# Kernel tuning notes

Measured on AMD Instinct MI355X. Metric: run time of the kernel, lower is better.

Reference implementation:

```python
import jax, jax.numpy as jnp
import numpy as np

B, T, F, D, NCLS = 32, 1024, 128, 64, 11
EPS = 1e-3  # keras BatchNormalization default epsilon


def sinusoidal_pe(t, f, dtype=jnp.float32):
    pos = jnp.arange(t, dtype=jnp.float32)[:, None]                      # [T,1]
    div = jnp.exp(-jnp.log(10000.0) * jnp.arange(0, f, 2, dtype=jnp.float32) / f)
    ang = pos * div                                                      # [T,F/2]
    pe = jnp.zeros((t, f), dtype=jnp.float32)
    pe = pe.at[:, 0::2].set(jnp.sin(ang)).at[:, 1::2].set(jnp.cos(ang))
    return pe.astype(dtype)


def setup_inputs() -> dict:
    key = jax.random.key(0)
    ks = jax.random.split(key, 18)
    s = 0.05
    return {
        "x": jax.random.normal(ks[0], (B, T, F), jnp.float32),
        "wq": jax.random.normal(ks[1], (F, D), jnp.float32) * s,
        "wk": jax.random.normal(ks[2], (F, D), jnp.float32) * s,
        "wv": jax.random.normal(ks[3], (F, D), jnp.float32) * s,
        "bn_a_gamma": jax.random.uniform(ks[4], (D,), jnp.float32, 0.5, 1.5),
        "bn_a_beta": jax.random.normal(ks[5], (D,), jnp.float32) * s,
        "bn_a_mean": jax.random.normal(ks[6], (D,), jnp.float32) * s,
        "bn_a_var": jax.random.uniform(ks[7], (D,), jnp.float32, 0.5, 1.5),
        "w0": jax.random.normal(ks[8], (D, 64), jnp.float32) * s,
        "b0": jax.random.normal(ks[9], (64,), jnp.float32) * s,
        "w1": jax.random.normal(ks[10], (F, 64), jnp.float32) * s,
        "b1": jax.random.normal(ks[11], (64,), jnp.float32) * s,
        "bn1_gamma": jax.random.uniform(ks[12], (128,), jnp.float32, 0.5, 1.5),
        "bn1_beta": jax.random.normal(ks[13], (128,), jnp.float32) * s,
        "bn1_mean": jax.random.normal(ks[14], (128,), jnp.float32) * s,
        "bn1_var": jax.random.uniform(ks[15], (128,), jnp.float32, 0.5, 1.5),
        "wd": jax.random.normal(ks[16], (128, NCLS), jnp.float32) * s,
        "bd": jax.random.normal(ks[17], (NCLS,), jnp.float32) * s,
    }


def _bn(h, gamma, beta, mean, var):
    # inference-mode batch norm over last axis
    return (h - mean) * (gamma * jax.lax.rsqrt(var + EPS)) + beta


def reference(x, wq, wk, wv, bn_a_gamma, bn_a_beta, bn_a_mean, bn_a_var,
              w0, b0, w1, b1, bn1_gamma, bn1_beta, bn1_mean, bn1_var, wd, bd):
    # AttentionLayer: positional encoding + single-head scaled dot-product attention
    xp = x + sinusoidal_pe(x.shape[1], x.shape[2], x.dtype)              # [B,T,F]
    q = jnp.einsum("btf,fd->btd", xp, wq)
    k = jnp.einsum("btf,fd->btd", xp, wk)
    v = jnp.einsum("btf,fd->btd", xp, wv)
    scores = jnp.einsum("bqd,bkd->bqk", q, k) / jnp.sqrt(jnp.float32(D))  # [B,T,T]
    attn = jax.nn.softmax(scores, axis=-1)
    x1 = jnp.einsum("bqk,bkd->bqd", attn, v)                             # [B,T,D]
    x1 = _bn(x1, bn_a_gamma, bn_a_beta, bn_a_mean, bn_a_var)
    # per-timestep heads (vectorized over T)
    out1 = jax.nn.relu(jnp.einsum("btd,de->bte", x1, w0) + b0)           # [B,T,64]
    out2 = jax.nn.relu(jnp.einsum("btf,fe->bte", x, w1) + b1)            # [B,T,64]
    h = jnp.concatenate([out1, out2], axis=-1)                           # [B,T,128]
    h = _bn(h, bn1_gamma, bn1_beta, bn1_mean, bn1_var)
    # dropout is identity in inference mode
    logits = jnp.einsum("bte,ec->btc", h, wd) + bd                       # [B,T,11]
    return jax.nn.softmax(logits, axis=-1)
```

## Files before the change

kernel.cpp:

```cpp
#include <hip/hip_runtime.h>
#include <math.h>

#define BB 32
#define TT 1024
#define FF 128
#define DD 64
#define NCLS 11
constexpr float kEps = 1e-3f;
constexpr int M = BB * TT;

typedef __attribute__((ext_vector_type(8))) short short8v;
typedef __attribute__((ext_vector_type(4))) short short4v;
typedef __attribute__((ext_vector_type(4))) float float4v;
typedef __attribute__((ext_vector_type(16))) float float16v;

__device__ __forceinline__ short f2bf(float f) {
  union { float f; unsigned u; } v; v.f = f;
  return (short)((v.u + 0x7FFFu + ((v.u >> 16) & 1u)) >> 16);
}
__device__ __forceinline__ float bf2f(short s) {
  union { unsigned u; float f; } v; v.u = ((unsigned)(unsigned short)s) << 16;
  return v.f;
}

__device__ __forceinline__ short8v pack_swap(
    float p0, float p1, float p2, float p3,
    float p4, float p5, float p6, float p7) {
  unsigned a0, a1, b0, b1;
  asm("v_cvt_pk_bf16_f32 %0, %1, %2" : "=v"(a0) : "v"(p0), "v"(p1));
  asm("v_cvt_pk_bf16_f32 %0, %1, %2" : "=v"(a1) : "v"(p2), "v"(p3));
  asm("v_cvt_pk_bf16_f32 %0, %1, %2" : "=v"(b0) : "v"(p4), "v"(p5));
  asm("v_cvt_pk_bf16_f32 %0, %1, %2" : "=v"(b1) : "v"(p6), "v"(p7));
  asm volatile("v_permlane32_swap_b32 %0, %1" : "+v"(a0), "+v"(b0));
  asm volatile("v_permlane32_swap_b32 %0, %1" : "+v"(a1), "+v"(b1));
  union { unsigned u[4]; short8v s; } r;
  r.u[0] = a0; r.u[1] = a1; r.u[2] = b0; r.u[3] = b1;
  return r.s;
}

__global__ __launch_bounds__(256) void prep_kernel(
    const float* __restrict__ wq, const float* __restrict__ wk,
    const float* __restrict__ wv, const float* __restrict__ w1,
    const float* __restrict__ w0, const float* __restrict__ b0,
    const float* __restrict__ bn_a_gamma, const float* __restrict__ bn_a_beta,
    const float* __restrict__ bn_a_mean, const float* __restrict__ bn_a_var,
    const float* __restrict__ bn1_gamma, const float* __restrict__ bn1_beta,
    const float* __restrict__ bn1_mean, const float* __restrict__ bn1_var,
    const float* __restrict__ wd, const float* __restrict__ bd,
    short* __restrict__ wT4,
    short* __restrict__ w0pT, float* __restrict__ b0p,
    short* __restrict__ wdpT, float* __restrict__ bdp,
    float* __restrict__ peq, float* __restrict__ pek, float* __restrict__ pev) {
  const int t = threadIdx.x;
  const int blk = blockIdx.x;

  if (blk >= 5) {
    __shared__ float peL[16][128];
    const int p = blk - 5;
    const int y = p >> 6;
    const int t0 = (p & 63) * 16;
#pragma unroll
    for (int i = 0; i < 8; ++i) {
      const int idx = t + i * 256;
      const int tr = idx >> 7, f = idx & 127;
      const float div = expf(-logf(10000.0f) * (float)(f & ~1) / (float)FF);
      const float ang = (float)(t0 + tr) * div;
      peL[tr][f] = (f & 1) ? cosf(ang) : sinf(ang);
    }
    __syncthreads();
    const float* w = (y == 0) ? wq : (y == 1) ? wk : wv;
    float* dst = (y == 0) ? peq : (y == 1) ? pek : pev;
    const int tr = t >> 4, dq = t & 15;
    float4 acc = {0.f, 0.f, 0.f, 0.f};
    for (int f = 0; f < FF; ++f) {
      const float pv = peL[tr][f];
      const float4 w4 = *(const float4*)&w[f * 64 + dq * 4];
      acc.x += pv * w4.x; acc.y += pv * w4.y;
      acc.z += pv * w4.z; acc.w += pv * w4.w;
    }
    *(float4*)&dst[(t0 + tr) * 64 + dq * 4] = acc;
    return;
  }
  if (blk > 0) {
    const int y = blk - 1;
    const float* w = (y == 0) ? wq : (y == 1) ? wk : (y == 2) ? wv : w1;
    short* dst = wT4 + y * 8192;
#pragma unroll
    for (int i = 0; i < 4; ++i) {
      const int idx = t + i * 256;
      const int n = idx >> 4, c = idx & 15;
      short8v s8;
#pragma unroll
      for (int j = 0; j < 8; ++j) s8[j] = f2bf(w[(c * 8 + j) * 64 + n]);
      *(short8v*)&dst[n * 128 + ((c ^ (n & 7)) << 3)] = s8;
    }
    return;
  }
  __shared__ float cA[64], cAo[64], c1s[64], c1o[64], c2s[64], c2o[64];
  if (t < 64) {
    const float sA = bn_a_gamma[t] * rsqrtf(bn_a_var[t] + kEps);
    cA[t] = sA; cAo[t] = bn_a_beta[t] - bn_a_mean[t] * sA;
    const float s1 = bn1_gamma[t] * rsqrtf(bn1_var[t] + kEps);
    c1s[t] = s1; c1o[t] = bn1_beta[t] - bn1_mean[t] * s1;
    const float s2 = bn1_gamma[t + 64] * rsqrtf(bn1_var[t + 64] + kEps);
    c2s[t] = s2; c2o[t] = bn1_beta[t + 64] - bn1_mean[t + 64] * s2;
  }
  __syncthreads();
  for (int i = t; i < 4096; i += 256) {
    const int e = i >> 6, k = i & 63;
    w0pT[i] = f2bf(cA[k] * w0[k * 64 + e]);
  }
  if (t < 64) {
    float s = b0[t];
    for (int k = 0; k < 64; ++k) s += cAo[k] * w0[k * 64 + t];
    b0p[t] = s;
  }
  for (int i = t; i < 2048; i += 256) {
    const int c = i >> 7, e = i & 127;
    float v = 0.f;
    if (c < NCLS) v = wd[e * NCLS + c] * (e < 64 ? c1s[e] : c2s[e - 64]);
    wdpT[i] = f2bf(v);
  }
  if (t < 16) {
    float s = 0.f;
    if (t < NCLS) {
      s = bd[t];
      for (int e = 0; e < 64; ++e) s += c1o[e] * wd[e * NCLS + t];
      for (int e = 0; e < 64; ++e) s += c2o[e] * wd[(64 + e) * NCLS + t];
    }
    bdp[t] = s;
  }
}

__global__ __launch_bounds__(256) void proj_kernel(
    const float* __restrict__ x, const short* __restrict__ wT4,
    const float* __restrict__ peq, const float* __restrict__ pek,
    const float* __restrict__ pev, const float* __restrict__ b1,
    short* __restrict__ qo, short* __restrict__ ko,
    short* __restrict__ vt, short* __restrict__ o2) {
  __shared__ __align__(16) short xs[128 * 128];
  __shared__ __align__(16) short wsh[64 * 128];
  const int tid = threadIdx.x;
  const int lane = tid & 63;
  const int wv4 = tid >> 6;
  const int l15 = lane & 15;
  const int lg = lane >> 4;
  const int r0 = blockIdx.x * 128;
  const int y = blockIdx.y;

#pragma unroll
  for (int i = 0; i < 8; ++i) {
    int id = tid + i * 256;
    int row = id >> 4, chunk = id & 15;
    const float* xp = &x[((size_t)(r0 + row)) * FF + chunk * 8];
    const float4 a = *(const float4*)xp;
    const float4 b = *(const float4*)(xp + 4);
    short8v s8;
    s8[0] = f2bf(a.x); s8[1] = f2bf(a.y); s8[2] = f2bf(a.z); s8[3] = f2bf(a.w);
    s8[4] = f2bf(b.x); s8[5] = f2bf(b.y); s8[6] = f2bf(b.z); s8[7] = f2bf(b.w);
    *(short8v*)&xs[row * 128 + ((chunk ^ (row & 7)) << 3)] = s8;
  }
#pragma unroll
  for (int i = 0; i < 4; ++i) {
    const int idx = tid + i * 256;
    *(int4*)&wsh[idx * 8] = *(const int4*)&wT4[y * 8192 + idx * 8];
  }
  __syncthreads();

  float4v acc[2][4];
#pragma unroll
  for (int rt = 0; rt < 2; ++rt)
#pragma unroll
    for (int dt = 0; dt < 4; ++dt) acc[rt][dt] = (float4v)0.0f;

  const bool natural = (y == 2);
#pragma unroll
  for (int kt = 0; kt < 4; ++kt) {
    const int chunk = kt * 4 + lg;
    short8v xa[2], wa[4];
#pragma unroll
    for (int rt = 0; rt < 2; ++rt) {
      const int row = wv4 * 32 + rt * 16 + l15;
      xa[rt] = *(const short8v*)&xs[row * 128 + ((chunk ^ (row & 7)) << 3)];
    }
#pragma unroll
    for (int dt = 0; dt < 4; ++dt) {
      const int n = dt * 16 + l15;
      wa[dt] = *(const short8v*)&wsh[n * 128 + ((chunk ^ (n & 7)) << 3)];
    }
#pragma unroll
    for (int rt = 0; rt < 2; ++rt)
#pragma unroll
      for (int dt = 0; dt < 4; ++dt)
        acc[rt][dt] = natural
            ? __builtin_amdgcn_mfma_f32_16x16x32_bf16(xa[rt], wa[dt], acc[rt][dt], 0, 0, 0)
            : __builtin_amdgcn_mfma_f32_16x16x32_bf16(wa[dt], xa[rt], acc[rt][dt], 0, 0, 0);
  }

  if (natural) {
    const int bq = r0 >> 10;
    const int tb = (r0 & 1023) + wv4 * 32;
#pragma unroll
    for (int rt = 0; rt < 2; ++rt) {
#pragma unroll
      for (int dt = 0; dt < 4; ++dt) {
        const int d = dt * 16 + l15;
        const int t0 = tb + rt * 16 + lg * 4;
        short4v s;
#pragma unroll
        for (int r = 0; r < 4; ++r)
          s[r] = f2bf(acc[rt][dt][r] + pev[(t0 + r) * 64 + d]);
        *(short4v*)&vt[((size_t)(bq * DD + d)) * TT + t0] = s;
      }
    }
  } else {
    short* dst = (y == 0) ? qo : (y == 1) ? ko : o2;
    const float* petab = (y == 0) ? peq : pek;
    const float qs = (y == 0) ? 0.18033688f : 1.0f;
#pragma unroll
    for (int rt = 0; rt < 2; ++rt) {
      const int row = r0 + wv4 * 32 + rt * 16 + l15;
      const int tr = row & 1023;
#pragma unroll
      for (int dt = 0; dt < 4; ++dt) {
        const int d0 = dt * 16 + lg * 4;
        float v0 = acc[rt][dt][0], v1 = acc[rt][dt][1];
        float v2 = acc[rt][dt][2], v3 = acc[rt][dt][3];
        if (y == 3) {
          const float4 bv = *(const float4*)&b1[d0];
          v0 = fmaxf(v0 + bv.x, 0.f); v1 = fmaxf(v1 + bv.y, 0.f);
          v2 = fmaxf(v2 + bv.z, 0.f); v3 = fmaxf(v3 + bv.w, 0.f);
        } else {
          const float4 pv = *(const float4*)&petab[tr * 64 + d0];
          v0 = (v0 + pv.x) * qs; v1 = (v1 + pv.y) * qs;
          v2 = (v2 + pv.z) * qs; v3 = (v3 + pv.w) * qs;
        }
        short4v s;
        s[0] = f2bf(v0); s[1] = f2bf(v1); s[2] = f2bf(v2); s[3] = f2bf(v3);
        *(short4v*)&dst[(size_t)row * DD + d0] = s;
      }
    }
  }
}

__global__ __launch_bounds__(512, 4) void attn_head_kernel(
    const short* __restrict__ qg, const short* __restrict__ kg,
    const short* __restrict__ vtg, const short* __restrict__ o2m,
    const short* __restrict__ w0pT, const float* __restrict__ b0p,
    const short* __restrict__ wdpT, const float* __restrict__ bdp,
    float* __restrict__ out) {
  __shared__ __align__(16) char LB[65536];
  const int tid = threadIdx.x;
  const int lane = tid & 63;
  const int wid = tid >> 6;
  const int qwv = wid & 1;
  const int grp = wid >> 1;
  const int id = blockIdx.x;
  const int bb = id & 31;
  const int qx = id >> 5;
  const int l31 = lane & 31;
  const int lhi = lane >> 5;
  const int l15 = lane & 15;
  const int lg = lane >> 4;
  const int qbase = qx * 64 + qwv * 32;
  const int kvbase = grp * 256;
  const int stid = tid & 127;

  short* const Kb[2] = {(short*)(LB + grp * 16384),
                        (short*)(LB + grp * 16384 + 4096)};
  short* const Vb[2] = {(short*)(LB + grp * 16384 + 8192),
                        (short*)(LB + grp * 16384 + 12288)};

  const int krow0 = stid >> 3, kc8 = (stid & 7) * 8;
  const int ksw0 = kc8 ^ ((krow0 & 7) << 3);
  const int krow1 = krow0 + 16;
  const int ksw1 = kc8 ^ ((krow1 & 7) << 3);
  const int vd0 = stid >> 2, vt4 = stid & 3;
  const int vsw0 = (vt4 ^ (vd0 & 3)) * 8;
  const int vd1 = vd0 + 32;
  const int vsw1 = (vt4 ^ (vd1 & 3)) * 8;

  short8v qf[4];
#pragma unroll
  for (int dc = 0; dc < 4; ++dc)
    qf[dc] = *(const short8v*)&qg[((size_t)(bb * TT + qbase + l31)) * DD + dc * 16 + lhi * 8];

  float16v oacc[2];
  oacc[0] = (float16v)0.f; oacc[1] = (float16v)0.f;
  float lacc = 0.f;

  {
    *(int4*)&Kb[0][krow0 * 64 + ksw0] =
        *(const int4*)&kg[((size_t)(bb * TT + kvbase + krow0)) * DD + kc8];
    *(int4*)&Kb[0][krow1 * 64 + ksw1] =
        *(const int4*)&kg[((size_t)(bb * TT + kvbase + krow1)) * DD + kc8];
    *(int4*)&Vb[0][vd0 * 32 + vsw0] =
        *(const int4*)&vtg[((size_t)(bb * DD + vd0)) * TT + kvbase + vt4 * 8];
    *(int4*)&Vb[0][vd1 * 32 + vsw1] =
        *(const int4*)&vtg[((size_t)(bb * DD + vd1)) * TT + kvbase + vt4 * 8];
  }
  __syncthreads();

  for (int i = 0; i < 8; ++i) {
    const int cur = i & 1;
    short* const Kc = Kb[cur];
    short* const Vc = Vb[cur];

    int4 nk0, nk1, nv0, nv1;
    if (i < 7) {
      const int nkv = kvbase + (i + 1) * 32;
      nk0 = *(const int4*)&kg[((size_t)(bb * TT + nkv + krow0)) * DD + kc8];
      nk1 = *(const int4*)&kg[((size_t)(bb * TT + nkv + krow1)) * DD + kc8];
      nv0 = *(const int4*)&vtg[((size_t)(bb * DD + vd0)) * TT + nkv + vt4 * 8];
      nv1 = *(const int4*)&vtg[((size_t)(bb * DD + vd1)) * TT + nkv + vt4 * 8];
    }

    short8v kf[4];
#pragma unroll
    for (int dc = 0; dc < 4; ++dc) {
      const int chunk = (dc * 2 + lhi) ^ (l31 & 7);
      kf[dc] = *(const short8v*)&Kc[l31 * 64 + chunk * 8];
    }
    float16v s = (float16v)0.f;
#pragma unroll
    for (int dc = 0; dc < 4; ++dc)
      s = __builtin_amdgcn_mfma_f32_32x32x16_bf16(kf[dc], qf[dc], s, 0, 0, 0);

    float16v p;
#pragma unroll
    for (int r = 0; r < 16; ++r) { p[r] = exp2f(s[r]); lacc += p[r]; }

    const short8v pfa = pack_swap(p[0], p[1], p[2], p[3], p[4], p[5], p[6], p[7]);
    const short8v pfb = pack_swap(p[8], p[9], p[10], p[11], p[12], p[13], p[14], p[15]);

#pragma unroll
    for (int dh = 0; dh < 2; ++dh) {
      const int drow = dh * 32 + l31;
      const int c0 = (lhi) ^ (drow & 3);
      const int c1 = (2 + lhi) ^ (drow & 3);
      const short8v vf0 = *(const short8v*)&Vc[drow * 32 + c0 * 8];
      const short8v vf1 = *(const short8v*)&Vc[drow * 32 + c1 * 8];
      oacc[dh] = __builtin_amdgcn_mfma_f32_32x32x16_bf16(pfa, vf0, oacc[dh], 0, 0, 0);
      oacc[dh] = __builtin_amdgcn_mfma_f32_32x32x16_bf16(pfb, vf1, oacc[dh], 0, 0, 0);
    }

    if (i < 7) {
      short* const Kn = Kb[cur ^ 1];
      short* const Vn = Vb[cur ^ 1];
      *(int4*)&Kn[krow0 * 64 + ksw0] = nk0;
      *(int4*)&Kn[krow1 * 64 + ksw1] = nk1;
      *(int4*)&Vn[vd0 * 32 + vsw0] = nv0;
      *(int4*)&Vn[vd1 * 32 + vsw1] = nv1;
      __syncthreads();
    }
  }

  lacc += __shfl_xor(lacc, 32);

  __syncthreads();
  if (grp > 0) {
    float* cb = (float*)(LB + (grp - 1) * 16384);
#pragma unroll
    for (int dh = 0; dh < 2; ++dh)
#pragma unroll
      for (int r = 0; r < 16; ++r) {
        const int q = (r & 3) + 8 * (r >> 2) + 4 * lhi;
        cb[qwv * 2048 + q * 64 + dh * 32 + l31] = oacc[dh][r];
      }
    float* lcb = (float*)(LB + 49152);
    if (lhi == 0) lcb[(grp - 1) * 64 + qwv * 32 + l31] = lacc;
  }
  __syncthreads();
  if (grp == 0) {
#pragma unroll
    for (int g = 1; g < 4; ++g) {
      const float* cb = (const float*)(LB + (g - 1) * 16384);
#pragma unroll
      for (int dh = 0; dh < 2; ++dh)
#pragma unroll
        for (int r = 0; r < 16; ++r) {
          const int q = (r & 3) + 8 * (r >> 2) + 4 * lhi;
          oacc[dh][r] += cb[qwv * 2048 + q * 64 + dh * 32 + l31];
        }
    }
    const float* lcb = (const float*)(LB + 49152);
#pragma unroll
    for (int g = 1; g < 4; ++g) lacc += lcb[(g - 1) * 64 + qwv * 32 + l31];
    const float linv = 1.0f / lacc;

    short* hs = (short*)(LB + 50176 + qwv * 4096);
#pragma unroll
    for (int dh = 0; dh < 2; ++dh)
#pragma unroll
      for (int r = 0; r < 16; ++r) {
        const int q = (r & 3) + 8 * (r >> 2) + 4 * lhi;
        const int d = dh * 32 + l31;
        const int chunk = d >> 3;
        hs[q * 64 + ((chunk ^ (q & 7)) << 3) + (l31 & 7)] = f2bf(oacc[dh][r]);
      }

#pragma unroll
    for (int sub = 0; sub < 2; ++sub) {
      short* hsub = hs + sub * 16 * 64;
      short8v af[2];
#pragma unroll
      for (int dt = 0; dt < 2; ++dt) {
        const int chunk = (dt * 4 + lg) ^ (l15 & 7);
        af[dt] = *(const short8v*)&hsub[l15 * 64 + chunk * 8];
      }

      float4v acc1[4];
#pragma unroll
      for (int et = 0; et < 4; ++et) acc1[et] = (float4v)0.0f;
#pragma unroll
      for (int et = 0; et < 4; ++et)
#pragma unroll
        for (int dt = 0; dt < 2; ++dt) {
          const short8v wb = *(const short8v*)&w0pT[(et * 16 + l15) * 64 + dt * 32 + lg * 8];
          acc1[et] = __builtin_amdgcn_mfma_f32_16x16x32_bf16(af[dt], wb, acc1[et], 0, 0, 0);
        }

      float b0v[4];
#pragma unroll
      for (int et = 0; et < 4; ++et) b0v[et] = b0p[et * 16 + l15];

#pragma unroll
      for (int r = 0; r < 4; ++r) {
        const float invm = __shfl(linv, sub * 16 + lg * 4 + r);
        const int m = lg * 4 + r;
#pragma unroll
        for (int et = 0; et < 4; ++et) {
          const float v = fmaxf(acc1[et][r] * invm + b0v[et], 0.f);
          const int chunk = (et * 2 + (l15 >> 3)) ^ (m & 7);
          hsub[m * 64 + chunk * 8 + (l15 & 7)] = f2bf(v);
        }
      }

      float4v accL = (float4v)0.0f;
#pragma unroll
      for (int dt = 0; dt < 2; ++dt) {
        const int chunk = (dt * 4 + lg) ^ (l15 & 7);
        const short8v ha = *(const short8v*)&hsub[l15 * 64 + chunk * 8];
        const short8v wb = *(const short8v*)&wdpT[l15 * 128 + dt * 32 + lg * 8];
        accL = __builtin_amdgcn_mfma_f32_16x16x32_bf16(ha, wb, accL, 0, 0, 0);
      }
      const size_t o2row = ((size_t)bb * TT + qbase + sub * 16 + l15) * DD;
#pragma unroll
      for (int dt = 0; dt < 2; ++dt) {
        const short8v ha = *(const short8v*)&o2m[o2row + dt * 32 + lg * 8];
        const short8v wb = *(const short8v*)&wdpT[l15 * 128 + 64 + dt * 32 + lg * 8];
        accL = __builtin_amdgcn_mfma_f32_16x16x32_bf16(ha, wb, accL, 0, 0, 0);
      }

      const float bdv = bdp[l15];
#pragma unroll
      for (int r = 0; r < 4; ++r) {
        const float lv = (l15 < NCLS) ? (accL[r] + bdv) : -1e30f;
        float mx = lv;
#pragma unroll
        for (int off = 1; off < 16; off <<= 1) mx = fmaxf(mx, __shfl_xor(mx, off));
        const float ex = (l15 < NCLS) ? __expf(lv - mx) : 0.f;
        float sm = ex;
#pragma unroll
        for (int off = 1; off < 16; off <<= 1) sm += __shfl_xor(sm, off);
        if (l15 < NCLS)
          out[((size_t)bb * TT + qbase + sub * 16 + lg * 4 + r) * NCLS + l15] = ex / sm;
      }
    }
  }
}

extern "C" void kernel_launch(void* const* d_in, const int* in_sizes, int n_in,
                              void* d_out, int out_size, void* d_ws, size_t ws_size,
                              hipStream_t stream) {
  (void)in_sizes; (void)n_in; (void)out_size; (void)ws_size;
  const float* x  = (const float*)d_in[0];
  const float* wq = (const float*)d_in[1];
  const float* wk = (const float*)d_in[2];
  const float* wv = (const float*)d_in[3];
  const float* bn_a_gamma = (const float*)d_in[4];
  const float* bn_a_beta  = (const float*)d_in[5];
  const float* bn_a_mean  = (const float*)d_in[6];
  const float* bn_a_var   = (const float*)d_in[7];
  const float* w0 = (const float*)d_in[8];
  const float* b0 = (const float*)d_in[9];
  const float* w1 = (const float*)d_in[10];
  const float* b1 = (const float*)d_in[11];
  const float* bn1_gamma = (const float*)d_in[12];
  const float* bn1_beta  = (const float*)d_in[13];
  const float* bn1_mean  = (const float*)d_in[14];
  const float* bn1_var   = (const float*)d_in[15];
  const float* wd = (const float*)d_in[16];
  const float* bd = (const float*)d_in[17];
  float* out = (float*)d_out;

  char* cur = (char*)d_ws;
  short* q  = (short*)cur; cur += (size_t)M * DD * 2;
  short* k  = (short*)cur; cur += (size_t)M * DD * 2;
  short* vt = (short*)cur; cur += (size_t)M * DD * 2;
  short* o2 = (short*)cur; cur += (size_t)M * DD * 2;
  short* wT4  = (short*)cur; cur += 4 * 8192 * 2;
  short* w0pT = (short*)cur; cur += 4096 * 2;
  short* wdpT = (short*)cur; cur += 2048 * 2;
  float* b0p  = (float*)cur; cur += 64 * 4;
  float* bdp  = (float*)cur; cur += 16 * 4;
  float* peq  = (float*)cur; cur += (size_t)TT * DD * 4;
  float* pek  = (float*)cur; cur += (size_t)TT * DD * 4;
  float* pev  = (float*)cur; cur += (size_t)TT * DD * 4;

  prep_kernel<<<dim3(197), dim3(256), 0, stream>>>(
      wq, wk, wv, w1, w0, b0, bn_a_gamma, bn_a_beta, bn_a_mean, bn_a_var,
      bn1_gamma, bn1_beta, bn1_mean, bn1_var, wd, bd,
      wT4, w0pT, b0p, wdpT, bdp, peq, pek, pev);
  proj_kernel<<<dim3(M / 128, 4), dim3(256), 0, stream>>>(
      x, wT4, peq, pek, pev, b1, q, k, vt, o2);
  attn_head_kernel<<<dim3(512), dim3(512), 0, stream>>>(
      q, k, vt, o2, w0pT, b0p, wdpT, bdp, out);
}
```

Measured before the change: 54.51 us.

## Pre-convert x to bf16 once in prep kernel; add MFMA priority hints in attention

Adds 256 blocks to the prep kernel that convert the whole fp32 input x to a bf16 workspace buffer. The projection kernel, which previously re-read and re-converted fp32 x in each of its four y-slices, now loads bf16 rows directly, halving its x read traffic. In exchange there is an extra full write and read of a bf16 copy of x. Separately, the attention inner loop interleaves LDS loads with MFMAs, reuses the score registers for probabilities, and wraps the MFMA sections in s_setprio to favour matrix issue across waves.

```diff
diff --git a/kernel.cpp b/kernel.cpp
--- a/kernel.cpp
+++ b/kernel.cpp
@@ -39,6 +39,7 @@
 }
 
 __global__ __launch_bounds__(256) void prep_kernel(
+    const float* __restrict__ x,
     const float* __restrict__ wq, const float* __restrict__ wk,
     const float* __restrict__ wv, const float* __restrict__ w1,
     const float* __restrict__ w0, const float* __restrict__ b0,
@@ -47,13 +48,28 @@
     const float* __restrict__ bn1_gamma, const float* __restrict__ bn1_beta,
     const float* __restrict__ bn1_mean, const float* __restrict__ bn1_var,
     const float* __restrict__ wd, const float* __restrict__ bd,
-    short* __restrict__ wT4,
+    short* __restrict__ xbf, short* __restrict__ wT4,
     short* __restrict__ w0pT, float* __restrict__ b0p,
     short* __restrict__ wdpT, float* __restrict__ bdp,
     float* __restrict__ peq, float* __restrict__ pek, float* __restrict__ pev) {
   const int t = threadIdx.x;
   const int blk = blockIdx.x;
 
+  if (blk >= 197) {
+    const int p2 = blk - 197;
+    const size_t base = (size_t)p2 * 16384;
+#pragma unroll
+    for (int i = 0; i < 8; ++i) {
+      const size_t e0 = base + (size_t)i * 2048 + (size_t)t * 8;
+      const float4 a = *(const float4*)&x[e0];
+      const float4 b = *(const float4*)&x[e0 + 4];
+      short8v s8;
+      s8[0] = f2bf(a.x); s8[1] = f2bf(a.y); s8[2] = f2bf(a.z); s8[3] = f2bf(a.w);
+      s8[4] = f2bf(b.x); s8[5] = f2bf(b.y); s8[6] = f2bf(b.z); s8[7] = f2bf(b.w);
+      *(short8v*)&xbf[e0] = s8;
+    }
+    return;
+  }
   if (blk >= 5) {
     __shared__ float peL[16][128];
     const int p = blk - 5;
@@ -133,7 +149,7 @@
 }
 
 __global__ __launch_bounds__(256) void proj_kernel(
-    const float* __restrict__ x, const short* __restrict__ wT4,
+    const short* __restrict__ xbf, const short* __restrict__ wT4,
     const float* __restrict__ peq, const float* __restrict__ pek,
     const float* __restrict__ pev, const float* __restrict__ b1,
     short* __restrict__ qo, short* __restrict__ ko,
@@ -152,13 +168,8 @@
   for (int i = 0; i < 8; ++i) {
     int id = tid + i * 256;
     int row = id >> 4, chunk = id & 15;
-    const float* xp = &x[((size_t)(r0 + row)) * FF + chunk * 8];
-    const float4 a = *(const float4*)xp;
-    const float4 b = *(const float4*)(xp + 4);
-    short8v s8;
-    s8[0] = f2bf(a.x); s8[1] = f2bf(a.y); s8[2] = f2bf(a.z); s8[3] = f2bf(a.w);
-    s8[4] = f2bf(b.x); s8[5] = f2bf(b.y); s8[6] = f2bf(b.z); s8[7] = f2bf(b.w);
-    *(short8v*)&xs[row * 128 + ((chunk ^ (row & 7)) << 3)] = s8;
+    const int4 v = *(const int4*)&xbf[((size_t)(r0 + row)) * FF + chunk * 8];
+    *(int4*)&xs[row * 128 + ((chunk ^ (row & 7)) << 3)] = v;
   }
 #pragma unroll
   for (int i = 0; i < 4; ++i) {
@@ -315,34 +326,34 @@
       nv1 = *(const int4*)&vtg[((size_t)(bb * DD + vd1)) * TT + nkv + vt4 * 8];
     }
 
-    short8v kf[4];
+    float16v s = (float16v)0.f;
+    __builtin_amdgcn_s_setprio(1);
 #pragma unroll
     for (int dc = 0; dc < 4; ++dc) {
       const int chunk = (dc * 2 + lhi) ^ (l31 & 7);
-      kf[dc] = *(const short8v*)&Kc[l31 * 64 + chunk * 8];
-    }
-    float16v s = (float16v)0.f;
-#pragma unroll
-    for (int dc = 0; dc < 4; ++dc)
-      s = __builtin_amdgcn_mfma_f32_32x32x16_bf16(kf[dc], qf[dc], s, 0, 0, 0);
-
-    float16v p;
-#pragma unroll
-    for (int r = 0; r < 16; ++r) { p[r] = exp2f(s[r]); lacc += p[r]; }
-
-    const short8v pfa = pack_swap(p[0], p[1], p[2], p[3], p[4], p[5], p[6], p[7]);
-    const short8v pfb = pack_swap(p[8], p[9], p[10], p[11], p[12], p[13], p[14], p[15]);
-
+      const short8v kf = *(const short8v*)&Kc[l31 * 64 + chunk * 8];
+      s = __builtin_amdgcn_mfma_f32_32x32x16_bf16(kf, qf[dc], s, 0, 0, 0);
+    }
+    __builtin_amdgcn_s_setprio(0);
+
+#pragma unroll
+    for (int r = 0; r < 16; ++r) { s[r] = exp2f(s[r]); lacc += s[r]; }
+
+    const short8v pfa = pack_swap(s[0], s[1], s[2], s[3], s[4], s[5], s[6], s[7]);
+    const short8v pfb = pack_swap(s[8], s[9], s[10], s[11], s[12], s[13], s[14], s[15]);
+
+    __builtin_amdgcn_s_setprio(1);
 #pragma unroll
     for (int dh = 0; dh < 2; ++dh) {
       const int drow = dh * 32 + l31;
       const int c0 = (lhi) ^ (drow & 3);
+      const short8v vf0 = *(const short8v*)&Vc[drow * 32 + c0 * 8];
+      oacc[dh] = __builtin_amdgcn_mfma_f32_32x32x16_bf16(pfa, vf0, oacc[dh], 0, 0, 0);
       const int c1 = (2 + lhi) ^ (drow & 3);
-      const short8v vf0 = *(const short8v*)&Vc[drow * 32 + c0 * 8];
       const short8v vf1 = *(const short8v*)&Vc[drow * 32 + c1 * 8];
-      oacc[dh] = __builtin_amdgcn_mfma_f32_32x32x16_bf16(pfa, vf0, oacc[dh], 0, 0, 0);
       oacc[dh] = __builtin_amdgcn_mfma_f32_32x32x16_bf16(pfb, vf1, oacc[dh], 0, 0, 0);
     }
+    __builtin_amdgcn_s_setprio(0);
 
     if (i < 7) {
       short* const Kn = Kb[cur ^ 1];
@@ -499,6 +510,7 @@
   short* k  = (short*)cur; cur += (size_t)M * DD * 2;
   short* vt = (short*)cur; cur += (size_t)M * DD * 2;
   short* o2 = (short*)cur; cur += (size_t)M * DD * 2;
+  short* xbf = (short*)cur; cur += (size_t)M * FF * 2;
   short* wT4  = (short*)cur; cur += 4 * 8192 * 2;
   short* w0pT = (short*)cur; cur += 4096 * 2;
   short* wdpT = (short*)cur; cur += 2048 * 2;
@@ -508,12 +520,12 @@
   float* pek  = (float*)cur; cur += (size_t)TT * DD * 4;
   float* pev  = (float*)cur; cur += (size_t)TT * DD * 4;
 
-  prep_kernel<<<dim3(197), dim3(256), 0, stream>>>(
-      wq, wk, wv, w1, w0, b0, bn_a_gamma, bn_a_beta, bn_a_mean, bn_a_var,
+  prep_kernel<<<dim3(453), dim3(256), 0, stream>>>(
+      x, wq, wk, wv, w1, w0, b0, bn_a_gamma, bn_a_beta, bn_a_mean, bn_a_var,
       bn1_gamma, bn1_beta, bn1_mean, bn1_var, wd, bd,
-      wT4, w0pT, b0p, wdpT, bdp, peq, pek, pev);
+      xbf, wT4, w0pT, b0p, wdpT, bdp, peq, pek, pev);
   proj_kernel<<<dim3(M / 128, 4), dim3(256), 0, stream>>>(
-      x, wT4, peq, pek, pev, b1, q, k, vt, o2);
+      xbf, wT4, peq, pek, pev, b1, q, k, vt, o2);
   attn_head_kernel<<<dim3(512), dim3(512), 0, stream>>>(
       q, k, vt, o2, w0pT, b0p, wdpT, bdp, out);
 }
```

After: 53.04 us. -2.7%, faster.
